# Kernel optimization log

Measured on AMD Instinct MI355X. Metric: run time of the kernel, lower is better.

## Reference

```python
import jax, jax.numpy as jnp
import numpy as np


def setup_inputs() -> dict:
    key = jax.random.key(0)
    xyz = jax.random.normal(key, (16, 3, 4096), dtype=jnp.float32)  # (B,3,N), NCHW
    return {"xyz": xyz}


def _chamfer_means(a, b):
    # a: (B,N,3), b: (B,M,3); squared-distance chamfer, return per-batch means
    a2 = jnp.sum(a * a, axis=-1)            # (B,N)
    b2 = jnp.sum(b * b, axis=-1)            # (B,M)
    ab = jnp.einsum('bnd,bmd->bnm', a, b)   # (B,N,M)
    d2 = a2[:, :, None] + b2[:, None, :] - 2.0 * ab  # (B,N,M)
    dist12 = jnp.min(d2, axis=2)            # (B,N) nearest in b for each a
    dist21 = jnp.min(d2, axis=1)            # (B,M) nearest in a for each b
    return jnp.mean(dist12, axis=-1), jnp.mean(dist21, axis=-1)


def reference(xyz):
    # SymmetryLoss with sym_plane=('yz',): mirror x-coordinate (dim 0 of channel axis)
    mult = jnp.array([-1.0, 1.0, 1.0], dtype=xyz.dtype).reshape(1, 3, 1)
    m_xyz = jax.lax.stop_gradient(xyz * mult)   # mirrored points are detached
    a = jnp.transpose(m_xyz, (0, 2, 1))         # (B,N,3) generated (mirrored)
    b = jnp.transpose(xyz, (0, 2, 1))           # (B,N,3) reference
    mean12, mean21 = _chamfer_means(a, b)
    # LabeledChamferDistance with beta=0, gamma=1, delta=0:
    # loss = mean_b[ mean(dist12) + gamma * mean(dist21) ]
    loss = jnp.mean(mean12 + mean21)
    return loss
```

## Files before the change

### kernel.cpp

```cpp
#include <hip/hip_runtime.h>

#define BATCH 16
#define NPTS 4096
#define TOTN (BATCH * NPTS)
#define MH 4
#define MC (NPTS / MH)

typedef _Float16 f16;
typedef __attribute__((ext_vector_type(8))) _Float16 f16x8;
typedef __attribute__((ext_vector_type(16))) float f32x16;

__device__ __forceinline__ unsigned pk(f16 a, f16 b) {
    union { f16 h[2]; unsigned u; } t;
    t.h[0] = a; t.h[1] = b;
    return t.u;
}

__device__ __forceinline__ float min3f(float a, float b, float c) {
    return fminf(fminf(a, b), c);
}

__device__ __forceinline__ float treemin(const f32x16& d, float acc) {
    float t0 = min3f(d[0], d[1], d[2]);
    float t1 = min3f(d[3], d[4], d[5]);
    float t2 = min3f(d[6], d[7], d[8]);
    float t3 = min3f(d[9], d[10], d[11]);
    float t4 = min3f(d[12], d[13], d[14]);
    float u0 = min3f(t0, t1, t2);
    float u1 = min3f(t3, t4, d[15]);
    return min3f(acc, u0, u1);
}

__global__ __launch_bounds__(256, 4) void chamfer_mfma_kernel(
    const float* __restrict__ xyz, float* __restrict__ partials,
    float* __restrict__ out) {
    __shared__ uint4 T0[MC];
    __shared__ uint4 T1[MC];

    const int tid = threadIdx.x;
    if (blockIdx.x == 0 && tid == 0) out[0] = 0.0f;

    const int lane = tid & 63;
    const int wid = tid >> 6;
    const int lm = lane & 31;
    const int kh = lane >> 5;

    const int mh = blockIdx.x & (MH - 1);
    const int nsup = (blockIdx.x >> 2) & 15;
    const int b = blockIdx.x >> 6;
    const float* base = xyz + (size_t)b * 3 * NPTS;

    const int m0 = mh * MC;
    for (int i = tid; i < MC; i += 256) {
        int mg = m0 + i;
        float x = base[mg], y = base[NPTS + mg], z = base[2 * NPTS + mg];
        float cx = -2.f * x, cy = -2.f * y, cz = -2.f * z;
        float b2 = fmaf(x, x, fmaf(y, y, z * z));
        f16 cxh = (f16)cx, cxl = (f16)(cx - (float)cxh);
        f16 cyh = (f16)cy, cyl = (f16)(cy - (float)cyh);
        f16 czh = (f16)cz, czl = (f16)(cz - (float)czh);
        f16 b2h = (f16)b2, b2l = (f16)(b2 - (float)b2h);
        T0[i] = make_uint4(pk(cxh, cxh), pk(cxl, cyh), pk(cyh, cyl), pk(czh, czh));
        T1[i] = make_uint4(pk(czl, b2h), pk(b2l, (f16)0.f), 0u, 0u);
    }
    __syncthreads();

    const int n0 = nsup * 256 + wid * 64;
    f16x8 Bf[2];
#pragma unroll
    for (int tile = 0; tile < 2; ++tile) {
        int n = n0 + tile * 32 + lm;
        float ax = -base[n];
        float ay = base[NPTS + n];
        float az = base[2 * NPTS + n];
        f16 axh = (f16)ax, axl = (f16)(ax - (float)axh);
        f16 ayh = (f16)ay, ayl = (f16)(ay - (float)ayh);
        f16 azh = (f16)az, azl = (f16)(az - (float)azh);
        union { unsigned u[4]; f16x8 v; } B;
        if (kh == 0) {
            B.u[0] = pk(axh, axl); B.u[1] = pk(axh, ayh);
            B.u[2] = pk(ayl, ayh); B.u[3] = pk(azh, azl);
        } else {
            B.u[0] = pk(azh, (f16)1.f); B.u[1] = pk((f16)1.f, (f16)0.f);
            B.u[2] = 0u; B.u[3] = 0u;
        }
        Bf[tile] = B.v;
    }

    const uint4* Ab = kh ? T1 : T0;
    float acc0 = 1e30f, acc1 = 1e30f;
    const f32x16 zero = {};

#pragma unroll 4
    for (int t = 0; t < MC / 32; ++t) {
        union { uint4 q; f16x8 v; } A;
        A.q = Ab[t * 32 + lm];
        f32x16 d0 = __builtin_amdgcn_mfma_f32_32x32x16_f16(A.v, Bf[0], zero, 0, 0, 0);
        f32x16 d1 = __builtin_amdgcn_mfma_f32_32x32x16_f16(A.v, Bf[1], zero, 0, 0, 0);
        acc0 = treemin(d0, acc0);
        acc1 = treemin(d1, acc1);
    }

    acc0 = fminf(acc0, __shfl_xor(acc0, 32, 64));
    acc1 = fminf(acc1, __shfl_xor(acc1, 32, 64));

    float* dst = partials + (size_t)mh * TOTN + b * NPTS + n0;
    dst[kh * 32 + lm] = kh ? acc1 : acc0;
}

__global__ __launch_bounds__(256) void combine_kernel(
    const float* __restrict__ xyz, const float* __restrict__ partials,
    float* __restrict__ out) {
    __shared__ float red[4];
    const int n0 = (blockIdx.x * 256 + threadIdx.x) * 4;
    float4 v = *reinterpret_cast<const float4*>(&partials[n0]);
#pragma unroll
    for (int s = 1; s < MH; ++s) {
        float4 p = *reinterpret_cast<const float4*>(&partials[(size_t)s * TOTN + n0]);
        v.x = fminf(v.x, p.x); v.y = fminf(v.y, p.y);
        v.z = fminf(v.z, p.z); v.w = fminf(v.w, p.w);
    }

    const int b = n0 >> 12;
    const int i = n0 & (NPTS - 1);
    const float* base = xyz + (size_t)b * 3 * NPTS;
    float4 xv = *reinterpret_cast<const float4*>(&base[i]);
    float4 yv = *reinterpret_cast<const float4*>(&base[NPTS + i]);
    float4 zv = *reinterpret_cast<const float4*>(&base[2 * NPTS + i]);

    float s0 = v.x + fmaf(xv.x, xv.x, fmaf(yv.x, yv.x, zv.x * zv.x));
    float s1 = v.y + fmaf(xv.y, xv.y, fmaf(yv.y, yv.y, zv.y * zv.y));
    float s2 = v.z + fmaf(xv.z, xv.z, fmaf(yv.z, yv.z, zv.z * zv.z));
    float s3 = v.w + fmaf(xv.w, xv.w, fmaf(yv.w, yv.w, zv.w * zv.w));
    float sum = (s0 + s1) + (s2 + s3);

#pragma unroll
    for (int off = 32; off; off >>= 1) sum += __shfl_down(sum, off, 64);
    if ((threadIdx.x & 63) == 0) red[threadIdx.x >> 6] = sum;
    __syncthreads();
    if (threadIdx.x == 0) {
        float bs = (red[0] + red[1]) + (red[2] + red[3]);
        atomicAdd(out, bs * (2.0f / (float)TOTN));
    }
}

extern "C" void kernel_launch(void* const* d_in, const int* in_sizes, int n_in,
                              void* d_out, int out_size, void* d_ws, size_t ws_size,
                              hipStream_t stream) {
    const float* xyz = (const float*)d_in[0];
    float* out = (float*)d_out;
    float* partials = (float*)d_ws;

    chamfer_mfma_kernel<<<BATCH * 16 * MH, 256, 0, stream>>>(xyz, partials, out);
    combine_kernel<<<TOTN / 1024, 256, 0, stream>>>(xyz, partials, out);
}
```

Before: 17.69 us.

## Fuse chamfer min and combine into one kernel with staged full-M loop

Replaces the M-split chamfer kernel plus combine kernel with a single kernel. Each wave now owns 32 query points, loops over all 4096 reference points in four staged LDS tiles, and prefetches the next stage into registers while computing the current one. The cross-block min and the partials buffer go away. The block reduces into the output with an atomic, and a tiny reset kernel zeroes the output. Grid drops from 1024 to 512 blocks and MFMA per A-load halves (one B tile instead of two), trading parallelism and LDS reuse for less launch and partials traffic.

```diff
diff --git a/kernel.cpp b/kernel.cpp
--- a/kernel.cpp
+++ b/kernel.cpp
@@ -3,8 +3,8 @@
 #define BATCH 16
 #define NPTS 4096
 #define TOTN (BATCH * NPTS)
-#define MH 4
-#define MC (NPTS / MH)
+#define STAGE 1024
+#define NSTAGE (NPTS / STAGE)
 
 typedef _Float16 f16;
 typedef __attribute__((ext_vector_type(8))) _Float16 f16x8;
@@ -31,48 +31,31 @@
     return min3f(acc, u0, u1);
 }
 
-__global__ __launch_bounds__(256, 4) void chamfer_mfma_kernel(
-    const float* __restrict__ xyz, float* __restrict__ partials,
-    float* __restrict__ out) {
-    __shared__ uint4 T0[MC];
-    __shared__ uint4 T1[MC];
+__global__ void reset_kernel(float* __restrict__ out) { out[0] = 0.0f; }
+
+__global__ __launch_bounds__(256) void fused_chamfer_kernel(
+    const float* __restrict__ xyz, float* __restrict__ out) {
+    __shared__ uint4 T0[STAGE];
+    __shared__ uint4 T1[STAGE];
+    __shared__ float red[4];
 
     const int tid = threadIdx.x;
-    if (blockIdx.x == 0 && tid == 0) out[0] = 0.0f;
-
     const int lane = tid & 63;
     const int wid = tid >> 6;
     const int lm = lane & 31;
     const int kh = lane >> 5;
 
-    const int mh = blockIdx.x & (MH - 1);
-    const int nsup = (blockIdx.x >> 2) & 15;
-    const int b = blockIdx.x >> 6;
+    const int b = blockIdx.x >> 5;
+    const int ng = blockIdx.x & 31;
     const float* base = xyz + (size_t)b * 3 * NPTS;
 
-    const int m0 = mh * MC;
-    for (int i = tid; i < MC; i += 256) {
-        int mg = m0 + i;
-        float x = base[mg], y = base[NPTS + mg], z = base[2 * NPTS + mg];
-        float cx = -2.f * x, cy = -2.f * y, cz = -2.f * z;
-        float b2 = fmaf(x, x, fmaf(y, y, z * z));
-        f16 cxh = (f16)cx, cxl = (f16)(cx - (float)cxh);
-        f16 cyh = (f16)cy, cyl = (f16)(cy - (float)cyh);
-        f16 czh = (f16)cz, czl = (f16)(cz - (float)czh);
-        f16 b2h = (f16)b2, b2l = (f16)(b2 - (float)b2h);
-        T0[i] = make_uint4(pk(cxh, cxh), pk(cxl, cyh), pk(cyh, cyl), pk(czh, czh));
-        T1[i] = make_uint4(pk(czl, b2h), pk(b2l, (f16)0.f), 0u, 0u);
-    }
-    __syncthreads();
-
-    const int n0 = nsup * 256 + wid * 64;
-    f16x8 Bf[2];
-#pragma unroll
-    for (int tile = 0; tile < 2; ++tile) {
-        int n = n0 + tile * 32 + lm;
-        float ax = -base[n];
-        float ay = base[NPTS + n];
-        float az = base[2 * NPTS + n];
+    const int n = ng * 128 + wid * 32 + lm;
+    const float ax = -base[n];
+    const float ay = base[NPTS + n];
+    const float az = base[2 * NPTS + n];
+    const float a2 = fmaf(ax, ax, fmaf(ay, ay, az * az));
+    f16x8 Bf;
+    {
         f16 axh = (f16)ax, axl = (f16)(ax - (float)axh);
         f16 ayh = (f16)ay, ayl = (f16)(ay - (float)ayh);
         f16 azh = (f16)az, azl = (f16)(az - (float)azh);
@@ -84,64 +67,61 @@
             B.u[0] = pk(azh, (f16)1.f); B.u[1] = pk((f16)1.f, (f16)0.f);
             B.u[2] = 0u; B.u[3] = 0u;
         }
-        Bf[tile] = B.v;
+        Bf = B.v;
     }
 
-    const uint4* Ab = kh ? T1 : T0;
-    float acc0 = 1e30f, acc1 = 1e30f;
+    float sx[4], sy[4], sz[4];
+#pragma unroll
+    for (int j = 0; j < 4; ++j) {
+        int mg = tid + j * 256;
+        sx[j] = base[mg]; sy[j] = base[NPTS + mg]; sz[j] = base[2 * NPTS + mg];
+    }
+
+    float acc = 1e30f;
     const f32x16 zero = {};
 
+    for (int s = 0; s < NSTAGE; ++s) {
+        __syncthreads();
+#pragma unroll
+        for (int j = 0; j < 4; ++j) {
+            int i = tid + j * 256;
+            float x = sx[j], y = sy[j], z = sz[j];
+            float cx = -2.f * x, cy = -2.f * y, cz = -2.f * z;
+            float b2 = fmaf(x, x, fmaf(y, y, z * z));
+            f16 cxh = (f16)cx, cxl = (f16)(cx - (float)cxh);
+            f16 cyh = (f16)cy, cyl = (f16)(cy - (float)cyh);
+            f16 czh = (f16)cz, czl = (f16)(cz - (float)czh);
+            f16 b2h = (f16)b2, b2l = (f16)(b2 - (float)b2h);
+            T0[i] = make_uint4(pk(cxh, cxh), pk(cxl, cyh), pk(cyh, cyl), pk(czh, czh));
+            T1[i] = make_uint4(pk(czl, b2h), pk(b2l, (f16)0.f), 0u, 0u);
+        }
+        __syncthreads();
+        if (s + 1 < NSTAGE) {
+#pragma unroll
+            for (int j = 0; j < 4; ++j) {
+                int mg = (s + 1) * STAGE + tid + j * 256;
+                sx[j] = base[mg]; sy[j] = base[NPTS + mg]; sz[j] = base[2 * NPTS + mg];
+            }
+        }
+
+        const uint4* Ab = kh ? T1 : T0;
 #pragma unroll 4
-    for (int t = 0; t < MC / 32; ++t) {
-        union { uint4 q; f16x8 v; } A;
-        A.q = Ab[t * 32 + lm];
-        f32x16 d0 = __builtin_amdgcn_mfma_f32_32x32x16_f16(A.v, Bf[0], zero, 0, 0, 0);
-        f32x16 d1 = __builtin_amdgcn_mfma_f32_32x32x16_f16(A.v, Bf[1], zero, 0, 0, 0);
-        acc0 = treemin(d0, acc0);
-        acc1 = treemin(d1, acc1);
+        for (int t = 0; t < STAGE / 32; ++t) {
+            union { uint4 q; f16x8 v; } A;
+            A.q = Ab[t * 32 + lm];
+            f32x16 d = __builtin_amdgcn_mfma_f32_32x32x16_f16(A.v, Bf, zero, 0, 0, 0);
+            acc = treemin(d, acc);
+        }
     }
 
-    acc0 = fminf(acc0, __shfl_xor(acc0, 32, 64));
-    acc1 = fminf(acc1, __shfl_xor(acc1, 32, 64));
-
-    float* dst = partials + (size_t)mh * TOTN + b * NPTS + n0;
-    dst[kh * 32 + lm] = kh ? acc1 : acc0;
-}
-
-__global__ __launch_bounds__(256) void combine_kernel(
-    const float* __restrict__ xyz, const float* __restrict__ partials,
-    float* __restrict__ out) {
-    __shared__ float red[4];
-    const int n0 = (blockIdx.x * 256 + threadIdx.x) * 4;
-    float4 v = *reinterpret_cast<const float4*>(&partials[n0]);
+    acc = fminf(acc, __shfl_xor(acc, 32, 64));
+    float val = (lane < 32) ? (acc + a2) : 0.0f;
 #pragma unroll
-    for (int s = 1; s < MH; ++s) {
-        float4 p = *reinterpret_cast<const float4*>(&partials[(size_t)s * TOTN + n0]);
-        v.x = fminf(v.x, p.x); v.y = fminf(v.y, p.y);
-        v.z = fminf(v.z, p.z); v.w = fminf(v.w, p.w);
-    }
-
-    const int b = n0 >> 12;
-    const int i = n0 & (NPTS - 1);
-    const float* base = xyz + (size_t)b * 3 * NPTS;
-    float4 xv = *reinterpret_cast<const float4*>(&base[i]);
-    float4 yv = *reinterpret_cast<const float4*>(&base[NPTS + i]);
-    float4 zv = *reinterpret_cast<const float4*>(&base[2 * NPTS + i]);
-
-    float s0 = v.x + fmaf(xv.x, xv.x, fmaf(yv.x, yv.x, zv.x * zv.x));
-    float s1 = v.y + fmaf(xv.y, xv.y, fmaf(yv.y, yv.y, zv.y * zv.y));
-    float s2 = v.z + fmaf(xv.z, xv.z, fmaf(yv.z, yv.z, zv.z * zv.z));
-    float s3 = v.w + fmaf(xv.w, xv.w, fmaf(yv.w, yv.w, zv.w * zv.w));
-    float sum = (s0 + s1) + (s2 + s3);
-
-#pragma unroll
-    for (int off = 32; off; off >>= 1) sum += __shfl_down(sum, off, 64);
-    if ((threadIdx.x & 63) == 0) red[threadIdx.x >> 6] = sum;
+    for (int off = 32; off; off >>= 1) val += __shfl_down(val, off, 64);
+    if (lane == 0) red[wid] = val;
     __syncthreads();
-    if (threadIdx.x == 0) {
-        float bs = (red[0] + red[1]) + (red[2] + red[3]);
-        atomicAdd(out, bs * (2.0f / (float)TOTN));
-    }
+    if (tid == 0)
+        atomicAdd(out, ((red[0] + red[1]) + (red[2] + red[3])) * (2.0f / (float)TOTN));
 }
 
 extern "C" void kernel_launch(void* const* d_in, const int* in_sizes, int n_in,
@@ -149,8 +129,7 @@
                               hipStream_t stream) {
     const float* xyz = (const float*)d_in[0];
     float* out = (float*)d_out;
-    float* partials = (float*)d_ws;
 
-    chamfer_mfma_kernel<<<BATCH * 16 * MH, 256, 0, stream>>>(xyz, partials, out);
-    combine_kernel<<<TOTN / 1024, 256, 0, stream>>>(xyz, partials, out);
+    reset_kernel<<<1, 1, 0, stream>>>(out);
+    fused_chamfer_kernel<<<BATCH * 32, 256, 0, stream>>>(xyz, out);
 }
```

Result: slower. 31.68 us (+79.1%).
